# Kernel optimization log

Hardware: AMD Instinct MI355X
Metric: run time of the kernel (lower is better)

## Reference

```python
import jax, jax.numpy as jnp
import numpy as np

T, B, D, H, NQ = 512, 256, 512, 512, 8  # time, batch, input_dim, hidden_dim, n_qubits


def setup_inputs() -> dict:
    key = jax.random.key(0)
    ks = jax.random.split(key, 11)
    rn = lambda k, shp, s=1.0: jax.random.normal(k, shp, dtype=jnp.float32) * s
    return {
        "inputs": rn(ks[0], (T, B, D)),
        # input_to_qubit: torch Linear(D+H, NQ) -> weight [NQ, D+H], bias [NQ]
        "W_itq": rn(ks[1], (NQ, D + H), 1.0 / np.sqrt(D + H)),
        "b_itq": rn(ks[2], (NQ,), 0.01),
        # per-gate Linear(NQ, NQ, bias=False) weight [NQ, NQ] and circuit params theta [NQ]
        "W_in": rn(ks[3], (NQ, NQ)), "th_in": rn(ks[4], (NQ,)),
        "W_fg": rn(ks[5], (NQ, NQ)), "th_fg": rn(ks[6], (NQ,)),
        "W_up": rn(ks[7], (NQ, NQ)), "th_up": rn(ks[8], (NQ,)),
        "W_out": rn(ks[9], (NQ, NQ)), "th_out": rn(ks[10], (NQ,)),
    }


def _gate(q, W, th):
    # x_qubit = q @ W.T ; circuit: RX(x_i) RY(th_i) per wire + CNOT chain, <Z_0>.
    # Z on wire 0 commutes with the CNOT chain, so <Z_0> = cos(x_0) * cos(th_0).
    x0 = q @ W[0]  # only wire 0 affects the expectation; [B]
    return jax.nn.sigmoid(jnp.cos(x0) * jnp.cos(th[0]))


def reference(inputs, W_itq, b_itq, W_in, th_in, W_fg, th_fg, W_up, th_up, W_out, th_out):
    b = inputs.shape[1]
    hx0 = jnp.zeros((b, H), inputs.dtype)
    cx0 = jnp.zeros((b, H), inputs.dtype)

    def step(carry, x):
        hx, cx = carry
        combined = jnp.concatenate([x, hx], axis=1)          # [B, D+H]
        q = combined @ W_itq.T + b_itq                        # [B, NQ]
        i = _gate(q, W_in, th_in)[:, None]                    # [B, 1]
        f = _gate(q, W_fg, th_fg)[:, None]
        g = _gate(q, W_up, th_up)[:, None]
        o = _gate(q, W_out, th_out)[:, None]
        cx = f * cx + i * g
        hx = o * jnp.tanh(cx)
        return (hx, cx), hx

    (hx, cx), ys = jax.lax.scan(step, (hx0, cx0), inputs)
    return ys, (hx, cx)
```

## Files before the change

### kernel.cpp

```cpp
#include <hip/hip_runtime.h>
#include <math.h>


constexpr int TT = 512;
constexpr int BB = 256;
constexpr int DD = 512;
constexpr int HH = 512;

__global__ void prep_kernel(const float* __restrict__ W_itq, const float* __restrict__ b_itq,
                            const float* __restrict__ W_in, const float* __restrict__ th_in,
                            const float* __restrict__ W_fg, const float* __restrict__ th_fg,
                            const float* __restrict__ W_up, const float* __restrict__ th_up,
                            const float* __restrict__ W_out, const float* __restrict__ th_out,
                            float* __restrict__ V, float* __restrict__ C) {
    int d = threadIdx.x;
    float vi = 0.f, vf = 0.f, vu = 0.f, vo = 0.f;
    #pragma unroll
    for (int n = 0; n < 8; ++n) {
        float w = W_itq[n * (DD + HH) + d];
        vi += w * W_in[n];
        vf += w * W_fg[n];
        vu += w * W_up[n];
        vo += w * W_out[n];
    }
    V[0 * DD + d] = vi;
    V[1 * DD + d] = vf;
    V[2 * DD + d] = vu;
    V[3 * DD + d] = vo;

    __shared__ float whsum[8];
    int wv = d >> 6, lane = d & 63;
    float s = 0.f;
    for (int h = lane; h < HH; h += 64) s += W_itq[wv * (DD + HH) + DD + h];
    #pragma unroll
    for (int off = 32; off > 0; off >>= 1) s += __shfl_down(s, off);
    if (lane == 0) whsum[wv] = s;
    __syncthreads();

    if (d < 4) {
        const float* Wg = (d == 0) ? W_in : (d == 1) ? W_fg : (d == 2) ? W_up : W_out;
        const float* th = (d == 0) ? th_in : (d == 1) ? th_fg : (d == 2) ? th_up : th_out;
        float c = 0.f, dg = 0.f;
        #pragma unroll
        for (int n = 0; n < 8; ++n) {
            c  += whsum[n] * Wg[n];
            dg += b_itq[n] * Wg[n];
        }
        C[d]     = c;
        C[4 + d] = cosf(th[0]);
        C[8 + d] = dg;
    }
}

__global__ void __launch_bounds__(256) proj_kernel(const float* __restrict__ x,
                                                   const float* __restrict__ V,
                                                   const float* __restrict__ C,
                                                   float* __restrict__ A) {
    int lane = threadIdx.x & 63;

    float4 v0[4], v1[4];
    #pragma unroll
    for (int g = 0; g < 4; ++g) {
        const float4* vg = (const float4*)(V + g * DD);
        v0[g] = vg[lane];
        v1[g] = vg[64 + lane];
    }
    float dg[4];
    #pragma unroll
    for (int g = 0; g < 4; ++g) dg[g] = C[8 + g];

    int wid = (int)((blockIdx.x * 256u + threadIdx.x) >> 6);
    int nw  = (int)((gridDim.x * 256u) >> 6);
    for (int r = wid; r < TT * BB; r += nw) {
        const float4* xr = (const float4*)(x + (size_t)r * DD);
        float4 a0 = xr[lane];
        float4 a1 = xr[64 + lane];
        float p[4];
        #pragma unroll
        for (int g = 0; g < 4; ++g) {
            p[g] = a0.x * v0[g].x + a0.y * v0[g].y + a0.z * v0[g].z + a0.w * v0[g].w
                 + a1.x * v1[g].x + a1.y * v1[g].y + a1.z * v1[g].z + a1.w * v1[g].w;
        }
        #pragma unroll
        for (int off = 32; off > 0; off >>= 1) {
            #pragma unroll
            for (int g = 0; g < 4; ++g) p[g] += __shfl_down(p[g], off);
        }
        if (lane == 0) {
            float4 o = make_float4(p[0] + dg[0], p[1] + dg[1], p[2] + dg[2], p[3] + dg[3]);
            ((float4*)A)[r] = o;
        }
    }
}

__global__ void scan_kernel(const float* __restrict__ A, const float* __restrict__ C,
                            float* __restrict__ hv, float* __restrict__ cfin) {
    int b = threadIdx.x;
    float c0 = C[0], c1 = C[1], c2 = C[2], c3 = C[3];
    float q0 = C[4], q1 = C[5], q2 = C[6], q3 = C[7];
    float hval = 0.f, cval = 0.f;
    const float4* A4 = (const float4*)A;
    #pragma unroll 2
    for (int t = 0; t < TT; ++t) {
        float4 a = A4[t * BB + b];
        float zi = __cosf(__fmaf_rn(hval, c0, a.x)) * q0;
        float zf = __cosf(__fmaf_rn(hval, c1, a.y)) * q1;
        float zu = __cosf(__fmaf_rn(hval, c2, a.z)) * q2;
        float zo = __cosf(__fmaf_rn(hval, c3, a.w)) * q3;
        float gi = __builtin_amdgcn_rcpf(1.f + __expf(-zi));
        float gf = __builtin_amdgcn_rcpf(1.f + __expf(-zf));
        float gu = __builtin_amdgcn_rcpf(1.f + __expf(-zu));
        float go = __builtin_amdgcn_rcpf(1.f + __expf(-zo));
        cval = __fmaf_rn(gf, cval, gi * gu);
        float e  = __expf(2.f * cval);
        float th = 1.f - 2.f * __builtin_amdgcn_rcpf(e + 1.f);
        hval = go * th;
        hv[t * BB + b] = hval;
    }
    cfin[b] = cval;
}

__global__ void __launch_bounds__(256) bcast_kernel(const float* __restrict__ hv,
                                                    const float* __restrict__ cfin,
                                                    float* __restrict__ out) {
    int wid  = (int)((blockIdx.x * 256u + threadIdx.x) >> 6);
    int lane = threadIdx.x & 63;
    int nw   = (int)((gridDim.x * 256u) >> 6);
    const int nrow = TT * BB + 2 * BB;
    for (int r = wid; r < nrow; r += nw) {
        float val;
        if (r < TT * BB)           val = hv[r];
        else if (r < TT * BB + BB) val = hv[(TT - 1) * BB + (r - TT * BB)];
        else                       val = cfin[r - TT * BB - BB];
        float4 v = make_float4(val, val, val, val);
        float4* o = (float4*)(out + (size_t)r * HH);
        o[lane]      = v;
        o[64 + lane] = v;
    }
}

extern "C" void kernel_launch(void* const* d_in, const int* in_sizes, int n_in,
                              void* d_out, int out_size, void* d_ws, size_t ws_size,
                              hipStream_t stream) {
    const float* x     = (const float*)d_in[0];
    const float* W_itq = (const float*)d_in[1];
    const float* b_itq = (const float*)d_in[2];
    const float* W_in  = (const float*)d_in[3];
    const float* th_in = (const float*)d_in[4];
    const float* W_fg  = (const float*)d_in[5];
    const float* th_fg = (const float*)d_in[6];
    const float* W_up  = (const float*)d_in[7];
    const float* th_up = (const float*)d_in[8];
    const float* W_out = (const float*)d_in[9];
    const float* th_out= (const float*)d_in[10];
    float* out = (float*)d_out;

    float* ws   = (float*)d_ws;
    float* V    = ws;
    float* C    = ws + 2048;
    float* A    = ws + 4096;
    float* hv   = A + TT * BB * 4;
    float* cfin = hv + TT * BB;

    prep_kernel<<<1, 512, 0, stream>>>(W_itq, b_itq, W_in, th_in, W_fg, th_fg,
                                       W_up, th_up, W_out, th_out, V, C);
    proj_kernel<<<2048, 256, 0, stream>>>(x, V, C, A);
    scan_kernel<<<1, BB, 0, stream>>>(A, C, hv, cfin);
    bcast_kernel<<<2048, 256, 0, stream>>>(hv, cfin, out);
}
```

Before: 591.0 us.

## Prefetch scan inputs eight steps ahead and split scan across four blocks

The sequential scan kernel now register-prefetches the next eight timesteps of projected gate inputs while it computes the current eight, which hides global load latency on the serial dependency chain. The batch is split across four single-wavefront blocks instead of one 256-thread block, so the work lands on several CUs. The sigmoid and tanh exponentials are rewritten as raw exp2 with the log2e and sign factors folded into the precomputed constants. This costs more registers, and the clamped prefetch past the end does a few redundant loads.

```diff
diff --git a/kernel.cpp b/kernel.cpp
--- a/kernel.cpp
+++ b/kernel.cpp
@@ -6,6 +6,9 @@
 constexpr int BB = 256;
 constexpr int DD = 512;
 constexpr int HH = 512;
+
+#define LOG2E 1.44269504088896340736f
+#define EXP2F(x) __builtin_amdgcn_exp2f(x)
 
 __global__ void prep_kernel(const float* __restrict__ W_itq, const float* __restrict__ b_itq,
                             const float* __restrict__ W_in, const float* __restrict__ th_in,
@@ -47,7 +50,7 @@
             dg += b_itq[n] * Wg[n];
         }
         C[d]     = c;
-        C[4 + d] = cosf(th[0]);
+        C[4 + d] = -cosf(th[0]) * LOG2E;
         C[8 + d] = dg;
     }
 }
@@ -93,29 +96,42 @@
     }
 }
 
-__global__ void scan_kernel(const float* __restrict__ A, const float* __restrict__ C,
-                            float* __restrict__ hv, float* __restrict__ cfin) {
-    int b = threadIdx.x;
+__global__ void __launch_bounds__(64, 1) scan_kernel(const float* __restrict__ A,
+                                                     const float* __restrict__ C,
+                                                     float* __restrict__ hv,
+                                                     float* __restrict__ cfin) {
+    int b = blockIdx.x * 64 + threadIdx.x;
     float c0 = C[0], c1 = C[1], c2 = C[2], c3 = C[3];
     float q0 = C[4], q1 = C[5], q2 = C[6], q3 = C[7];
     float hval = 0.f, cval = 0.f;
     const float4* A4 = (const float4*)A;
-    #pragma unroll 2
-    for (int t = 0; t < TT; ++t) {
-        float4 a = A4[t * BB + b];
-        float zi = __cosf(__fmaf_rn(hval, c0, a.x)) * q0;
-        float zf = __cosf(__fmaf_rn(hval, c1, a.y)) * q1;
-        float zu = __cosf(__fmaf_rn(hval, c2, a.z)) * q2;
-        float zo = __cosf(__fmaf_rn(hval, c3, a.w)) * q3;
-        float gi = __builtin_amdgcn_rcpf(1.f + __expf(-zi));
-        float gf = __builtin_amdgcn_rcpf(1.f + __expf(-zf));
-        float gu = __builtin_amdgcn_rcpf(1.f + __expf(-zu));
-        float go = __builtin_amdgcn_rcpf(1.f + __expf(-zo));
-        cval = __fmaf_rn(gf, cval, gi * gu);
-        float e  = __expf(2.f * cval);
-        float th = 1.f - 2.f * __builtin_amdgcn_rcpf(e + 1.f);
-        hval = go * th;
-        hv[t * BB + b] = hval;
+
+    float4 buf[8];
+    #pragma unroll
+    for (int j = 0; j < 8; ++j) buf[j] = A4[j * BB + b];
+
+    for (int tg = 0; tg < TT; tg += 8) {
+        float4 nxt[8];
+        #pragma unroll
+        for (int j = 0; j < 8; ++j) {
+            int tt = tg + 8 + j; if (tt > TT - 1) tt = TT - 1;
+            nxt[j] = A4[tt * BB + b];
+        }
+        #pragma unroll
+        for (int j = 0; j < 8; ++j) {
+            float4 a = buf[j];
+            float gi = __builtin_amdgcn_rcpf(1.f + EXP2F(__cosf(__fmaf_rn(hval, c0, a.x)) * q0));
+            float gf = __builtin_amdgcn_rcpf(1.f + EXP2F(__cosf(__fmaf_rn(hval, c1, a.y)) * q1));
+            float gu = __builtin_amdgcn_rcpf(1.f + EXP2F(__cosf(__fmaf_rn(hval, c2, a.z)) * q2));
+            float go = __builtin_amdgcn_rcpf(1.f + EXP2F(__cosf(__fmaf_rn(hval, c3, a.w)) * q3));
+            cval = __fmaf_rn(gf, cval, gi * gu);
+            float e  = EXP2F(cval * (2.f * LOG2E));
+            float th = __fmaf_rn(-2.f, __builtin_amdgcn_rcpf(e + 1.f), 1.f);
+            hval = go * th;
+            hv[(tg + j) * BB + b] = hval;
+        }
+        #pragma unroll
+        for (int j = 0; j < 8; ++j) buf[j] = nxt[j];
     }
     cfin[b] = cval;
 }
@@ -165,6 +181,6 @@
     prep_kernel<<<1, 512, 0, stream>>>(W_itq, b_itq, W_in, th_in, W_fg, th_fg,
                                        W_up, th_up, W_out, th_out, V, C);
     proj_kernel<<<2048, 256, 0, stream>>>(x, V, C, A);
-    scan_kernel<<<1, BB, 0, stream>>>(A, C, hv, cfin);
+    scan_kernel<<<4, 64, 0, stream>>>(A, C, hv, cfin);
     bcast_kernel<<<2048, 256, 0, stream>>>(hv, cfin, out);
 }
```

Result: faster. 534.5 us (-9.6%).
